# Optimization experiments

Hardware: AMD Instinct MI355X
Metric: run time of the kernel (lower is better)

Reference implementation:

```python
import jax, jax.numpy as jnp
import numpy as np

SE = 128        # num_sensors
T = 256         # timesteps
D_OB = 4        # d_ob_emb
D_PE = 16
D_STATIC = 64
B = 128
N_HEADS = 4
D_FF = 128
N_TRAN = 2
N_PROP = 2
N_CLASSES = 2
D_FEAT = T * D_OB              # 1024, prop-layer feature dim
D_MODEL = SE * D_OB + D_PE     # 528, transformer d_model
D_FINAL = D_MODEL + SE * D_OB  # 1040, mlp input (with static emb)
LN_EPS = 1e-5
NEG_INF = -1e9


def _layernorm(x, g, b):
    m = jnp.mean(x, axis=-1, keepdims=True)
    v = jnp.mean(jnp.square(x - m), axis=-1, keepdims=True)
    return (x - m) * jax.lax.rsqrt(v + LN_EPS) * g + b


def setup_inputs() -> dict:
    key = jax.random.key(0)
    ks = iter(jax.random.split(key, 40))

    def g(shape, scale=0.02):
        return jax.random.normal(next(ks), shape, jnp.float32) * scale

    a = float(np.sqrt(6.0 / (1 + SE * D_OB)))  # glorot for R_u
    inp = {
        'src': jax.random.normal(next(ks), (T, B, 2 * SE), jnp.float32),
        'times': jax.random.uniform(next(ks), (T, B), jnp.float32) * T,
        'lengths': jax.random.randint(next(ks), (B,), 1, T + 1),
        'static': jax.random.normal(next(ks), (B, D_STATIC), jnp.float32),
        'R_u': jax.random.uniform(next(ks), (1, SE * D_OB), jnp.float32, -a, a),
        'static_W': g((SE * D_OB, D_STATIC)),
        'static_b': g((SE * D_OB,)),
        'p_Wq': g((N_PROP, D_FEAT, D_FEAT)),
        'p_Wk': g((N_PROP, D_FEAT, D_FEAT)),
        'p_Wv': g((N_PROP, D_FEAT, D_FEAT)),
        'p_bq': g((N_PROP, D_FEAT)),
        'p_bk': g((N_PROP, D_FEAT)),
        'p_bv': g((N_PROP, D_FEAT)),
        'p_Wskip': g((N_PROP, D_FEAT, D_FEAT)),
        'p_bskip': g((N_PROP, D_FEAT)),
        't_Wqkv': g((N_TRAN, 3 * D_MODEL, D_MODEL)),
        't_bqkv': g((N_TRAN, 3 * D_MODEL)),
        't_Wo': g((N_TRAN, D_MODEL, D_MODEL)),
        't_bo': g((N_TRAN, D_MODEL)),
        't_W1': g((N_TRAN, D_FF, D_MODEL)),
        't_b1': g((N_TRAN, D_FF)),
        't_W2': g((N_TRAN, D_MODEL, D_FF)),
        't_b2': g((N_TRAN, D_MODEL)),
        't_ln1g': jnp.ones((N_TRAN, D_MODEL), jnp.float32),
        't_ln1b': jnp.zeros((N_TRAN, D_MODEL), jnp.float32),
        't_ln2g': jnp.ones((N_TRAN, D_MODEL), jnp.float32),
        't_ln2b': jnp.zeros((N_TRAN, D_MODEL), jnp.float32),
        'mlp_W1': g((D_FINAL, D_FINAL)),
        'mlp_b1': g((D_FINAL,)),
        'mlp_W2': g((N_CLASSES, D_FINAL)),
        'mlp_b2': g((N_CLASSES,)),
    }
    return inp


def reference(src, times, lengths, static, R_u, static_W, static_b,
              p_Wq, p_Wk, p_Wv, p_bq, p_bk, p_bv, p_Wskip, p_bskip,
              t_Wqkv, t_bqkv, t_Wo, t_bo, t_W1, t_b1, t_W2, t_b2,
              t_ln1g, t_ln1b, t_ln2g, t_ln2b,
              mlp_W1, mlp_b1, mlp_W2, mlp_b2):
    # --- positional encoding (PositionalEncodingTF): sin/cos of times over timescales ---
    ts = jnp.asarray(float(T)) ** jnp.linspace(0.0, 1.0, D_PE // 2)
    st = times[..., None] / ts                       # (T,B,D_PE//2)
    pe = jnp.concatenate([jnp.sin(st), jnp.cos(st)], axis=-1)  # (T,B,D_PE)

    static_emb = static @ static_W.T + static_b      # (B, SE*D_OB)

    # --- per-sensor observation embedding ---
    x = src[:, :, :SE]
    x = jnp.repeat(x, D_OB, axis=-1)                 # (T,B,SE*D_OB)
    h = jax.nn.relu(x * R_u)                         # dropout = identity (eval)

    # --- diagonalized graphs: each batch element is a fully-connected Se-node graph.
    # The block-diagonal edge list over B*Se*Se edges is equivalent to dense
    # batched attention (B, Se, Se); we honor that structure densely. ---
    hg = h.reshape(T, B, SE, D_OB).transpose(1, 2, 0, 3).reshape(B, SE, D_FEAT)
    W = jnp.ones((B, SE, SE), h.dtype)               # edge weights [b, tgt, src], adj=ones
    scale = 1.0 / jnp.sqrt(jnp.asarray(D_FEAT, h.dtype))
    for l in range(N_PROP):
        q = hg @ p_Wq[l].T + p_bq[l]
        k = hg @ p_Wk[l].T + p_bk[l]
        v = hg @ p_Wv[l].T + p_bv[l]
        scores = jnp.einsum('bid,bjd->bij', q, k) * scale   # i=target, j=source
        alpha = jax.nn.softmax(scores, axis=-1)              # softmax over sources
        hg = jnp.einsum('bij,bjd->bid', alpha * W, v) + hg @ p_Wskip[l].T + p_bskip[l]
        W = alpha                                            # attn weights feed next layer

    out = hg.reshape(B, SE, T, D_OB).transpose(2, 0, 1, 3).reshape(T, B, SE * D_OB)
    out = jnp.concatenate([out, pe], axis=2)          # (T,B,D_MODEL)

    # --- transformer encoder (post-norm, relu FF, key_padding_mask) ---
    time_mask = jnp.arange(T)[None, :] >= lengths[:, None]   # (B,T) True = pad
    hd = D_MODEL // N_HEADS
    xx = out
    for l in range(N_TRAN):
        qkv = xx @ t_Wqkv[l].T + t_bqkv[l]            # (T,B,3*D_MODEL)
        q, k, v = jnp.split(qkv, 3, axis=-1)
        def _heads(z):
            return z.reshape(T, B, N_HEADS, hd).transpose(1, 2, 0, 3)  # (B,H,T,hd)
        qh, kh, vh = _heads(q), _heads(k), _heads(v)
        att = jnp.einsum('bhqd,bhkd->bhqk', qh, kh) / jnp.sqrt(jnp.asarray(hd, xx.dtype))
        att = jnp.where(time_mask[:, None, None, :], NEG_INF, att)
        att = jax.nn.softmax(att, axis=-1)
        o = jnp.einsum('bhqk,bhkd->bhqd', att, vh).transpose(2, 0, 1, 3).reshape(T, B, D_MODEL)
        o = o @ t_Wo[l].T + t_bo[l]
        xx = _layernorm(xx + o, t_ln1g[l], t_ln1b[l])
        ff = jax.nn.relu(xx @ t_W1[l].T + t_b1[l]) @ t_W2[l].T + t_b2[l]
        xx = _layernorm(xx + ff, t_ln2g[l], t_ln2b[l])

    # --- masked mean pooling over time, static concat, MLP head ---
    keep = (~time_mask).astype(xx.dtype).T[:, :, None]        # (T,B,1)
    pooled = jnp.sum(xx * keep, axis=0) / (lengths[:, None].astype(xx.dtype) + 1.0)
    pooled = jnp.concatenate([pooled, static_emb], axis=1)    # (B, D_FINAL)
    hid = jax.nn.relu(pooled @ mlp_W1.T + mlp_b1)
    return hid @ mlp_W2.T + mlp_b2                            # (B, N_CLASSES)
```

## Files before the change

kernel.cpp:

```cpp
#include <hip/hip_runtime.h>
#include <hip/hip_bf16.h>
#include <math.h>

#define SE_    128
#define T_     256
#define B_     128
#define NH_    4
#define HD_    132
#define D_MODEL_ 528
#define D_FINAL_ 1040
#define D_FF_  128

typedef __hip_bfloat16 bf16;
typedef __attribute__((ext_vector_type(8))) short bf16x8v;
typedef __attribute__((ext_vector_type(4))) float f32x4;

__device__ __forceinline__ float bfb(unsigned short u){
  union { float f; unsigned int i; } c; c.i = ((unsigned int)u) << 16; return c.f;
}
__device__ __forceinline__ unsigned short bfr(float x){
  unsigned u = __builtin_bit_cast(unsigned, x);
  unsigned r = (u + 0x7FFFu + ((u >> 16) & 1u)) >> 16;
  return (unsigned short)r;
}
__device__ __forceinline__ void split1(float x, short& h, short& l){
  const unsigned short hu = bfr(x);
  const unsigned short lu = bfr(x - bfb(hu));
  h = (short)hu; l = (short)lu;
}
__device__ __forceinline__ float prd(const short* p, long i, long lo){
  return bfb((unsigned short)p[i]) + bfb((unsigned short)p[i+lo]);
}
__device__ __forceinline__ float rdIn(const void* p, long i, int f32){
  return f32 ? ((const float*)p)[i] : __bfloat162float(((const bf16*)p)[i]);
}

__global__ void detect_k(const void* __restrict__ src, int* __restrict__ flag){
  const unsigned int* p = (const unsigned int*)src;
  int bad = 0;
  for (int i = threadIdx.x; i < 4096; i += 256){
    const unsigned int lo = p[i] & 0xFFFFu;
    const unsigned int e = (lo >> 7) & 0xFFu;
    if (e >= 0xC0u) bad++;
  }
  __shared__ int red[256];
  red[threadIdx.x] = bad; __syncthreads();
  for (int h = 128; h > 0; h >>= 1){
    if (threadIdx.x < h) red[threadIdx.x] += red[threadIdx.x+h];
    __syncthreads();
  }
  if (threadIdx.x == 0) *flag = (red[0] > 64) ? 1 : 0;
}

#define MAXE 40
struct CvtTab {
  const void* src[MAXE];
  long srcOff[MAXE];
  long dstOff[MAXE];
  int n[MAXE];
  int bstart[MAXE];
  int cnt;
};
__global__ void cvt_all(CvtTab tb, short* __restrict__ wts, long loW, const int* __restrict__ flag){
  const int b = blockIdx.x;
  int e = 0;
  for (int i = 1; i < tb.cnt; ++i) if (tb.bstart[i] <= b) e = i;
  const long i = (long)(b - tb.bstart[e])*256 + threadIdx.x;
  if (i >= tb.n[e]) return;
  const float v = rdIn(tb.src[e], tb.srcOff[e] + i, *flag);
  short h, l; split1(v, h, l);
  wts[tb.dstOff[e] + i] = h;
  wts[tb.dstOff[e] + i + loW] = l;
}

struct RegsP { int4 v[4]; };

template<bool A16>
__device__ __forceinline__ void ld_pair(const short* __restrict__ P, long lo, long ld,
                                        int kb, int K, int g, bool valid, int sc0, RegsP& r){
  short* a = (short*)r.v;
  const int k0 = kb + sc0;
  const short* ph = P + (long)g*ld + k0;
  if (valid && (k0 + 16 <= K)){
    if (A16){
      r.v[0] = *(const int4*)(ph);
      r.v[1] = *(const int4*)(ph + 8);
      r.v[2] = *(const int4*)(ph + lo);
      r.v[3] = *(const int4*)(ph + lo + 8);
    } else {
      #pragma unroll
      for (int q=0;q<4;++q){
        *(int2*)(a + q*4)      = *(const int2*)(ph + q*4);
        *(int2*)(a + 16 + q*4) = *(const int2*)(ph + lo + q*4);
      }
    }
  } else {
    #pragma unroll
    for (int e2=0;e2<16;++e2){
      const bool ok = valid && (k0 + e2 < K);
      a[e2]    = ok ? ph[e2] : (short)0;
      a[16+e2] = ok ? ph[lo + e2] : (short)0;
    }
  }
}

__device__ __forceinline__ void ld_f32(const float* __restrict__ P, long ld, int kb, int K,
                                       int g, bool valid, int sc0, float* f){
  const int k0 = kb + sc0;
  const float* p = P + (long)g*ld + k0;
  if (valid && (k0 + 16 <= K)){
    #pragma unroll
    for (int q=0;q<4;++q) *(float4*)(f+q*4) = *(const float4*)(p + q*4);
  } else {
    #pragma unroll
    for (int e2=0;e2<16;++e2) f[e2] = (valid && (k0+e2) < K) ? p[e2] : 0.f;
  }
}

__device__ __forceinline__ void wr_pair(const RegsP& r, short* Lh, short* Ll, int srow, int sc0){
  *(int4*)(&Lh[srow*40 + sc0])     = r.v[0];
  *(int4*)(&Lh[srow*40 + sc0 + 8]) = r.v[1];
  *(int4*)(&Ll[srow*40 + sc0])     = r.v[2];
  *(int4*)(&Ll[srow*40 + sc0 + 8]) = r.v[3];
}
__device__ __forceinline__ void wr_split(const float* f, short* Lh, short* Ll, int srow, int sc0){
  short h[16], l[16];
  #pragma unroll
  for (int e2=0;e2<16;++e2) split1(f[e2], h[e2], l[e2]);
  *(int4*)(&Lh[srow*40+sc0])   = *(const int4*)(h);
  *(int4*)(&Lh[srow*40+sc0+8]) = *(const int4*)(h+8);
  *(int4*)(&Ll[srow*40+sc0])   = *(const int4*)(l);
  *(int4*)(&Ll[srow*40+sc0+8]) = *(const int4*)(l+8);
}

struct Route { short* C; long ldc; long lo; long sC; long sC2; int nEnd; int fl; };

template<bool SPLITA, bool A16>
__global__ __launch_bounds__(256) void gemm_s(
    const void* __restrict__ Ag, long loA,
    const short* __restrict__ Bg, long loB,
    const short* __restrict__ bias, long loBias,
    int M, int N, int K, long lda, long ldb,
    int nz1, long sA, long sB, long sA2, long sB2,
    int relu, int nroute, Route r0, Route r1, Route r2, float mult)
{
  __shared__ short As_h[128*40], As_l[128*40], Bs_h[128*40], Bs_l[128*40];
  const int tid = threadIdx.x;
  const int z1 = blockIdx.z % nz1, z2 = blockIdx.z / nz1;
  const int m0 = blockIdx.y*128, n0 = blockIdx.x*128;
  const void* A;
  if (SPLITA) A = (const void*)((const float*)Ag + z1*sA + z2*sA2);
  else        A = (const void*)((const short*)Ag + z1*sA + z2*sA2);
  const short* B = Bg + z1*sB + z2*sB2;
  short* Cb0 = r0.C + z1*r0.sC + z2*r0.sC2;
  short* Cb1 = (nroute > 1) ? (r1.C + z1*r1.sC + z2*r1.sC2) : nullptr;
  short* Cb2 = (nroute > 2) ? (r2.C + z1*r2.sC + z2*r2.sC2) : nullptr;

  const int srow = tid >> 1, sc0 = (tid & 1)*16;
  const int lane = tid & 63, wv = tid >> 6;
  const int wm = (wv >> 1)*64, wn = (wv & 1)*64;
  const int fr = lane & 15, kq = (lane >> 4)*8;

  const int gm_s = m0 + srow; const bool mval = gm_s < M;
  const int gn_s = n0 + srow; const bool nval = gn_s < N;

  RegsP rA, rB; float fA[16];
  if (SPLITA) ld_f32((const float*)A, lda, 0, K, gm_s, mval, sc0, fA);
  else        ld_pair<A16>((const short*)A, loA, lda, 0, K, gm_s, mval, sc0, rA);
  ld_pair<A16>(B, loB, ldb, 0, K, gn_s, nval, sc0, rB);

  f32x4 acc[4][4] = {};
  for (int kb = 0; kb < K; kb += 32){
    if (SPLITA) wr_split(fA, As_h, As_l, srow, sc0);
    else        wr_pair(rA, As_h, As_l, srow, sc0);
    wr_pair(rB, Bs_h, Bs_l, srow, sc0);
    __syncthreads();
    const int kn = kb + 32;
    if (kn < K){
      if (SPLITA) ld_f32((const float*)A, lda, kn, K, gm_s, mval, sc0, fA);
      else        ld_pair<A16>((const short*)A, loA, lda, kn, K, gm_s, mval, sc0, rA);
      ld_pair<A16>(B, loB, ldb, kn, K, gn_s, nval, sc0, rB);
    }
    bf16x8v ah[4], al[4], bh[4], bl[4];
    #pragma unroll
    for (int i=0;i<4;++i){
      ah[i] = *reinterpret_cast<const bf16x8v*>(&As_h[(wm + i*16 + fr)*40 + kq]);
      al[i] = *reinterpret_cast<const bf16x8v*>(&As_l[(wm + i*16 + fr)*40 + kq]);
      bh[i] = *reinterpret_cast<const bf16x8v*>(&Bs_h[(wn + i*16 + fr)*40 + kq]);
      bl[i] = *reinterpret_cast<const bf16x8v*>(&Bs_l[(wn + i*16 + fr)*40 + kq]);
    }
    #pragma unroll
    for (int i=0;i<4;++i)
      #pragma unroll
      for (int j=0;j<4;++j){
        acc[i][j] = __builtin_amdgcn_mfma_f32_16x16x32_bf16(ah[i], bh[j], acc[i][j], 0,0,0);
        acc[i][j] = __builtin_amdgcn_mfma_f32_16x16x32_bf16(ah[i], bl[j], acc[i][j], 0,0,0);
        acc[i][j] = __builtin_amdgcn_mfma_f32_16x16x32_bf16(al[i], bh[j], acc[i][j], 0,0,0);
      }
    __syncthreads();
  }

  const int cr = (lane >> 4)*4, cc = lane & 15;
  #pragma unroll
  for (int i=0;i<4;++i){
    #pragma unroll
    for (int j=0;j<4;++j){
      #pragma unroll
      for (int rr=0;rr<4;++rr){
        const int gm = m0 + wm + i*16 + cr + rr;
        const int gn = n0 + wn + j*16 + cc;
        if (gm < M && gn < N){
          float v = acc[i][j][rr] * mult;
          if (bias) v += prd(bias, gn, loBias);
          if (relu) v = fmaxf(v, 0.f);
          short* Cp; long ldc, lo; int fl, cn;
          if (nroute > 1 && gn >= r0.nEnd){
            if (nroute > 2 && gn >= r1.nEnd){ Cp=Cb2; ldc=r2.ldc; lo=r2.lo; fl=r2.fl; cn=gn-r1.nEnd; }
            else                            { Cp=Cb1; ldc=r1.ldc; lo=r1.lo; fl=r1.fl; cn=gn-r0.nEnd; }
          } else                            { Cp=Cb0; ldc=r0.ldc; lo=r0.lo; fl=r0.fl; cn=gn; }
          const long idx = (fl & 1) ? ((long)cn*ldc + gm) : ((long)gm*ldc + cn);
          if (fl & 2) v += prd(Cp, idx, lo);
          short h, l; split1(v, h, l);
          Cp[idx] = h; Cp[idx + lo] = l;
        }
      }
    }
  }
}

template<int NN, bool A16>
__global__ __launch_bounds__(256) void gemm_sm(
    const short* __restrict__ Ag, long loA, const short* __restrict__ Bg, long loB,
    int K, long lda, long ldb,
    int nz1, long sA, long sB, long sA2, long sB2,
    float* __restrict__ Sg, long sS, long sS2, int ldS,
    float mult, const int* __restrict__ lengths, int b0,
    const float* __restrict__ mulP, long sMul)
{
  __shared__ short As_h[128*40], As_l[128*40], Bs_h[128*40], Bs_l[128*40];
  const int tid = threadIdx.x;
  const int z1 = blockIdx.z % nz1, z2 = blockIdx.z / nz1;
  const int m0 = blockIdx.y*128;
  const short* A = Ag + z1*sA + z2*sA2;
  const short* B = Bg + z1*sB + z2*sB2;
  float* S = Sg + z1*sS + z2*sS2;

  const int srow = tid >> 1, sc0 = (tid & 1)*16;
  const int lane = tid & 63, wv = tid >> 6;
  const int wm = (wv >> 1)*64, wn = (wv & 1)*64;
  const int fr = lane & 15, kq = (lane >> 4)*8;
  const int cr = (lane >> 4)*4, cc = lane & 15;

  for (int nh = 0; nh < NN; nh += 128){
    RegsP rA, rB;
    ld_pair<A16>(A, loA, lda, 0, K, m0+srow, true, sc0, rA);
    ld_pair<A16>(B, loB, ldb, 0, K, nh+srow, true, sc0, rB);
    f32x4 acc[4][4] = {};
    for (int kb = 0; kb < K; kb += 32){
      wr_pair(rA, As_h, As_l, srow, sc0);
      wr_pair(rB, Bs_h, Bs_l, srow, sc0);
      __syncthreads();
      const int kn = kb + 32;
      if (kn < K){
        ld_pair<A16>(A, loA, lda, kn, K, m0+srow, true, sc0, rA);
        ld_pair<A16>(B, loB, ldb, kn, K, nh+srow, true, sc0, rB);
      }
      bf16x8v ah[4], al[4], bh[4], bl[4];
      #pragma unroll
      for (int i=0;i<4;++i){
        ah[i] = *reinterpret_cast<const bf16x8v*>(&As_h[(wm + i*16 + fr)*40 + kq]);
        al[i] = *reinterpret_cast<const bf16x8v*>(&As_l[(wm + i*16 + fr)*40 + kq]);
        bh[i] = *reinterpret_cast<const bf16x8v*>(&Bs_h[(wn + i*16 + fr)*40 + kq]);
        bl[i] = *reinterpret_cast<const bf16x8v*>(&Bs_l[(wn + i*16 + fr)*40 + kq]);
      }
      #pragma unroll
      for (int i=0;i<4;++i)
        #pragma unroll
        for (int j=0;j<4;++j){
          acc[i][j] = __builtin_amdgcn_mfma_f32_16x16x32_bf16(ah[i], bh[j], acc[i][j], 0,0,0);
          acc[i][j] = __builtin_amdgcn_mfma_f32_16x16x32_bf16(ah[i], bl[j], acc[i][j], 0,0,0);
          acc[i][j] = __builtin_amdgcn_mfma_f32_16x16x32_bf16(al[i], bh[j], acc[i][j], 0,0,0);
        }
      __syncthreads();
    }
    #pragma unroll
    for (int i=0;i<4;++i)
      #pragma unroll
      for (int j=0;j<4;++j)
        #pragma unroll
        for (int rr=0;rr<4;++rr){
          const int gm = m0 + wm + i*16 + cr + rr;
          const int gn = nh + wn + j*16 + cc;
          S[(long)gm*ldS + gn] = acc[i][j][rr] * mult;
        }
  }
  __syncthreads();

  constexpr int CH = NN / 64;
  const int cbase = lane*CH;
  int lim = NN;
  if (lengths){ const int L = lengths[b0 + z1]; lim = (L < NN) ? L : NN; }

  float v[CH], vn[CH], mcur[CH], mnxt[CH];
  {
    float* row0 = S + (long)(m0 + wv*32)*ldS + cbase;
    #pragma unroll
    for (int e=0;e<CH;++e) v[e] = row0[e];
    if (mulP){
      const float* mr = mulP + z1*sMul + (long)(m0 + wv*32)*ldS + cbase;
      #pragma unroll
      for (int e=0;e<CH;++e) mcur[e] = mr[e];
    }
  }
  for (int i = 0; i < 32; ++i){
    if (i < 31){
      float* rn = S + (long)(m0 + wv*32 + i + 1)*ldS + cbase;
      #pragma unroll
      for (int e=0;e<CH;++e) vn[e] = rn[e];
      if (mulP){
        const float* mr = mulP + z1*sMul + (long)(m0 + wv*32 + i + 1)*ldS + cbase;
        #pragma unroll
        for (int e=0;e<CH;++e) mnxt[e] = mr[e];
      }
    }
    float mx = -3.0e38f;
    #pragma unroll
    for (int e=0;e<CH;++e) if (cbase+e < lim) mx = fmaxf(mx, v[e]);
    #pragma unroll
    for (int o=32;o>0;o>>=1) mx = fmaxf(mx, __shfl_xor(mx, o, 64));
    float sm = 0.f;
    #pragma unroll
    for (int e=0;e<CH;++e){
      v[e] = (cbase+e < lim) ? __expf(v[e] - mx) : 0.f;
      sm += v[e];
    }
    #pragma unroll
    for (int o=32;o>0;o>>=1) sm += __shfl_xor(sm, o, 64);
    const float inv = 1.f / sm;
    float* row = S + (long)(m0 + wv*32 + i)*ldS + cbase;
    if (mulP){
      #pragma unroll
      for (int e=0;e<CH;++e) row[e] = v[e]*inv*mcur[e];
    } else {
      #pragma unroll
      for (int e=0;e<CH;++e) row[e] = v[e]*inv;
    }
    #pragma unroll
    for (int e=0;e<CH;++e){ v[e] = vn[e]; mcur[e] = mnxt[e]; }
  }
}

__global__ void build_hg(const void* __restrict__ src, const short* __restrict__ Ru, long loW,
                         short* __restrict__ hg, long loH, const int* __restrict__ flag, int b0){
  const int t = blockIdx.x, bl = blockIdx.y, se = threadIdx.x;
  const int f32 = *flag;
  const float s = rdIn(src, ((long)t*B_ + (b0+bl))*(2*SE_) + se, f32);
  const long o = ((long)bl*SE_ + se)*1024 + t*4;
  #pragma unroll
  for (int j=0;j<4;++j){
    const float v = fmaxf(s * prd(Ru, se*4+j, loW), 0.f);
    short h, l; split1(v, h, l);
    hg[o+j] = h; hg[o+j+loH] = l;
  }
}

__global__ void build_xx(const short* __restrict__ hg, long loH,
                         const short* __restrict__ times, long loW,
                         short* __restrict__ xx, long loX, int b0, int G){
  const int blk = blockIdx.x;
  const int t = blk / G, bl = blk % G, b = b0 + bl;
  const int tid = threadIdx.x;
  const float tm = prd(times, (long)t*B_ + b, loW);
  for (int c = tid; c < D_MODEL_; c += 256){
    float v;
    if (c < SE_*4){
      v = prd(hg, ((long)bl*SE_ + (c>>2))*1024 + t*4 + (c&3), loH);
    } else {
      const int p = c - SE_*4;
      const int i = p & 7;
      const float ts = exp2f(8.0f * (float)i / 7.0f);
      const float st = tm / ts;
      v = (p < 8) ? sinf(st) : cosf(st);
    }
    short h, l; split1(v, h, l);
    const long o = ((long)t*B_ + b)*D_MODEL_ + c;
    xx[o] = h; xx[o+loX] = l;
  }
}

__device__ __forceinline__ void ln_body_p(short* px, long loX, const short* pr, long loR,
                                          const short* g, const short* bb, long loW, int tid){
  const float x0 = prd(px,tid,loX)     + prd(pr,tid,loR);
  const float x1 = prd(px,tid+256,loX) + prd(pr,tid+256,loR);
  const float x2 = (tid < 16) ? (prd(px,tid+512,loX) + prd(pr,tid+512,loR)) : 0.f;
  __shared__ float rs[256], rq[256];
  rs[tid] = x0 + x1 + x2;
  rq[tid] = x0*x0 + x1*x1 + x2*x2;
  __syncthreads();
  for (int h = 128; h > 0; h >>= 1){
    if (tid < h){ rs[tid] += rs[tid+h]; rq[tid] += rq[tid+h]; }
    __syncthreads();
  }
  const float mean = rs[0] * (1.0f/528.0f);
  const float var  = rq[0] * (1.0f/528.0f) - mean*mean;
  const float inv = rsqrtf(var + 1e-5f);
  short h, l;
  split1((x0-mean)*inv*prd(g,tid,loW) + prd(bb,tid,loW), h, l);
  px[tid] = h; px[tid+loX] = l;
  split1((x1-mean)*inv*prd(g,tid+256,loW) + prd(bb,tid+256,loW), h, l);
  px[tid+256] = h; px[tid+256+loX] = l;
  if (tid < 16){
    split1((x2-mean)*inv*prd(g,tid+512,loW) + prd(bb,tid+512,loW), h, l);
    px[tid+512] = h; px[tid+512+loX] = l;
  }
}

__global__ __launch_bounds__(256) void ln_res_attn(short* __restrict__ xx, long loX,
    const short* __restrict__ res, long loR,
    const short* __restrict__ g, const short* __restrict__ bb, long loW, int b0){
  const int z = blockIdx.x >> 8, t = blockIdx.x & 255;
  short* px = xx + ((long)t*B_ + b0 + z)*D_MODEL_;
  const short* pr = res + (long)blockIdx.x*D_MODEL_;
  ln_body_p(px, loX, pr, loR, g, bb, loW, threadIdx.x);
}

__global__ __launch_bounds__(256) void ln_res_rows(short* __restrict__ xx, long loX,
    const short* __restrict__ res, long loR,
    const short* __restrict__ g, const short* __restrict__ bb, long loW, int r0){
  short* px = xx + ((long)r0 + blockIdx.x)*D_MODEL_;
  const short* pr = res + (long)blockIdx.x*D_MODEL_;
  ln_body_p(px, loX, pr, loR, g, bb, loW, threadIdx.x);
}

__global__ void pool_k(const short* __restrict__ xx, long loX, const int* __restrict__ len,
                       short* __restrict__ pooled, long loP){
  const int b = blockIdx.y;
  const int c = blockIdx.x*256 + threadIdx.x;
  if (c >= D_MODEL_) return;
  const int L = len[b];
  float s = 0.f;
  for (int t = 0; t < L; ++t) s += prd(xx, ((long)t*B_ + b)*D_MODEL_ + c, loX);
  short h, l; split1(s / (float)(L + 1), h, l);
  pooled[(long)b*D_FINAL_ + c] = h;
  pooled[(long)b*D_FINAL_ + c + loP] = l;
}

__global__ void logits_k(const short* __restrict__ hid, long loH,
                         const short* __restrict__ W2, const short* __restrict__ b2, long loW,
                         void* __restrict__ out, const int* __restrict__ flag){
  const int z = blockIdx.x;
  const int b = z >> 1, c = z & 1;
  const int lane = threadIdx.x;
  float s = 0.f;
  for (int k = lane; k < D_FINAL_; k += 64)
    s += prd(hid, (long)b*D_FINAL_ + k, loH) * prd(W2, (long)c*D_FINAL_ + k, loW);
  #pragma unroll
  for (int o = 32; o > 0; o >>= 1) s += __shfl_down(s, o, 64);
  if (lane == 0){
    const float r = s + prd(b2, c, loW);
    if (*flag) ((float*)out)[z] = r;
    else       ((bf16*)out)[z] = __float2bfloat16(r);
  }
}

extern "C" void kernel_launch(void* const* d_in, const int* in_sizes, int n_in,
                              void* d_out, int out_size, void* d_ws, size_t ws_size,
                              hipStream_t stream) {
  const int* lengths = (const int*)d_in[2];
  char* ws = (char*)d_ws;
  const size_t KB = 1024;

  short* wtsH = (short*)ws;
  int* flag = (int*)(ws + 47500*KB);
  short* xxH = (short*)(ws + 48000*KB);
  const long loXX = 17301504;
  char* SC = ws + 115600*KB;

  short* hgA = (short*)(SC + 0*KB);      const long loHG = 2097152;
  short* hgB = (short*)(SC + 8192*KB);
  short* qkc = (short*)(SC + 16384*KB);  const long loQK1 = 4194304;
  short* VtS = (short*)(SC + 32768*KB);  const long loVT1 = 2097152;
  float* S0c = (float*)(SC + 40960*KB);
  float* S1c = (float*)(SC + 41984*KB);
  short* qkb = (short*)(SC + 0*KB);      const long loQK2 = 4325376;
  short* o_c = (short*)(SC + 0*KB);      const long loOC  = 2162688;
  short* pjb = (short*)(SC + 8448*KB);   const long loPJ  = 2162688;
  short* vtb = (short*)(SC + 16896*KB);  const long loVT2 = 2162688;
  float* att = (float*)(SC + 25344*KB);
  short* ff1 = (short*)(SC + 0*KB);      const long loFF  = 4194304;
  short* pj2 = (short*)(SC + 16896*KB);  const long loPJ2 = 4325376;
  short* pooled = (short*)(SC + 0*KB);   const long loPO  = 133120;
  short* hid    = (short*)(SC + 1024*KB);

  CvtTab tb; long cur = 0; int nb = 0; int e = 0;
  auto add = [&](int idx, long so, long n)->long{
    tb.src[e] = d_in[idx]; tb.srcOff[e] = so; tb.dstOff[e] = cur;
    tb.n[e] = (int)n; tb.bstart[e] = nb;
    nb += (int)((n + 255)/256); cur += n; e++;
    return cur - n;
  };
  const long oT  = add(1,0,32768);
  const long oSt = add(3,0,8192);
  const long oRu = add(4,0,512);
  const long oSW = add(5,0,32768);
  const long oSb = add(6,0,512);
  long oQKSV[2], oBQ[2];
  for (int l = 0; l < 2; ++l){
    oQKSV[l] = add(7, (long)l*1048576, 1048576);
    add(8,  (long)l*1048576, 1048576);
    add(13, (long)l*1048576, 1048576);
    add(9,  (long)l*1048576, 1048576);
  }
  for (int l = 0; l < 2; ++l){
    oBQ[l] = add(10, (long)l*1024, 1024);
    add(11, (long)l*1024, 1024);
    add(14, (long)l*1024, 1024);
    add(12, (long)l*1024, 1024);
  }
  const long oWqkv = add(15,0,1672704);
  const long obqkv = add(16,0,3168);
  const long oWo = add(17,0,557568);
  const long obo = add(18,0,1056);
  const long oW1 = add(19,0,135168);
  const long ob1 = add(20,0,256);
  const long oW2 = add(21,0,135168);
  const long ob2 = add(22,0,1056);
  const long og1 = add(23,0,1056);
  const long obb1 = add(24,0,1056);
  const long og2 = add(25,0,1056);
  const long obb2 = add(26,0,1056);
  const long oM1 = add(27,0,1081600);
  const long oM1b = add(28,0,1040);
  const long oM2 = add(29,0,2080);
  const long oM2b = add(30,0,2);
  tb.cnt = e;
  const long loW = (cur + 7) & ~7L;

  detect_k<<<1,256,0,stream>>>(d_in[0], flag);
  cvt_all<<<nb,256,0,stream>>>(tb, wtsH, loW, flag);

  const Route RZ{nullptr,0,0,0,0,0,0};

  const int G1 = 16;
  for (int b0 = 0; b0 < B_; b0 += G1){
    build_hg<<<dim3(T_, G1), 128, 0, stream>>>(d_in[0], wtsH+oRu, loW, hgA, loHG, flag, b0);
    short* curb = hgA; short* nxtb = hgB;
    for (int l = 0; l < 2; ++l){
      float* S = (l == 0) ? S0c : S1c;
      {
        Route q{qkc, 2048, loQK1, 0, 0, 2048, 0};
        Route s{nxtb, 1024, loHG, 0, 0, 3072, 0};
        Route v{VtS, 2048, loVT1, 0, 0, 4096, 1};
        gemm_s<false,true><<<dim3(32,16,1),256,0,stream>>>(
            curb, loHG, wtsH+oQKSV[l], loW, wtsH+oBQ[l], loW,
            2048, 4096, 1024, 1024, 1024,
            1, 0,0,0,0, 0, 3, q, s, v, 1.f);
      }
      gemm_sm<128,true><<<dim3(1,1,G1),256,0,stream>>>(
          qkc, loQK1, qkc+1024, loQK1,
          1024, 2048, 2048,
          G1, 262144, 262144, 0, 0,
          S, 16384, 0, 128,
          0.03125f, nullptr, 0,
          (l == 1) ? S0c : nullptr, 16384);
      {
        Route c{nxtb, 1024, loHG, 131072, 0, 1024, 2};
        gemm_s<true,true><<<dim3(8,1,G1),256,0,stream>>>(
            S, 0, VtS, loVT1, nullptr, 0,
            128, 1024, 128, 128, 2048,
            G1, 16384, 128, 0, 0, 0, 1, c, RZ, RZ, 1.f);
      }
      short* t_ = curb; curb = nxtb; nxtb = t_;
    }
    build_xx<<<T_*G1,256,0,stream>>>(curb, loHG, wtsH+oT, loW, xxH, loXX, b0, G1);
  }

  const float iscl = 1.0f / sqrtf((float)HD_);
  const int G2 = 16;
  for (int l = 0; l < 2; ++l){
    const long wqkv = oWqkv + (long)l*836352;
    const long bqkv = obqkv + (long)l*1584;
    for (int b0 = 0; b0 < B_; b0 += G2){
      {
        Route qk{qkb, 1056, loQK2, 270336, 0, 1056, 0};
        Route v{vtb, 256, loVT2, 135168, 0, 1584, 1};
        gemm_s<false,true><<<dim3(13,2,G2),256,0,stream>>>(
            xxH + (long)b0*D_MODEL_, loXX, wtsH+wqkv, loW, wtsH+bqkv, loW,
            256, 1584, 528, (long)B_*D_MODEL_, 528,
            G2, 528, 0, 0, 0, 0, 2, qk, v, RZ, 1.f);
      }
      gemm_sm<256,false><<<dim3(1,2,G2*NH_),256,0,stream>>>(
          qkb, loQK2, qkb+528, loQK2,
          132, 1056, 1056,
          G2, 270336, 270336, 132, 132,
          att, 262144, 65536, 256,
          iscl, lengths, b0, nullptr, 0);
      {
        Route c{o_c, 528, loOC, 135168, 132, HD_, 0};
        gemm_s<true,true><<<dim3(2,2,G2*NH_),256,0,stream>>>(
            att, 0, vtb, loVT2, nullptr, 0,
            256, HD_, 256, 256, 256,
            G2, 262144, 135168, 65536, 33792, 0, 1, c, RZ, RZ, 1.f);
      }
      {
        Route c{pjb, 528, loPJ, 135168, 0, 528, 0};
        gemm_s<false,true><<<dim3(5,2,G2),256,0,stream>>>(
            o_c, loOC, wtsH+oWo+(long)l*278784, loW, wtsH+obo+(long)l*528, loW,
            256, 528, 528, 528, 528,
            G2, 135168, 0, 0, 0, 0, 1, c, RZ, RZ, 1.f);
      }
      ln_res_attn<<<G2*256,256,0,stream>>>(xxH, loXX, pjb, loPJ,
          wtsH+og1+(long)l*528, wtsH+obb1+(long)l*528, loW, b0);
    }
    {
      Route c{ff1, 128, loFF, 0, 0, 128, 0};
      gemm_s<false,true><<<dim3(1,256,1),256,0,stream>>>(
          xxH, loXX, wtsH+oW1+(long)l*67584, loW, wtsH+ob1+(long)l*128, loW,
          32768, 128, 528, 528, 528,
          1, 0,0,0,0, 1, 1, c, RZ, RZ, 1.f);
    }
    for (int r0 = 0; r0 < 32768; r0 += 8192){
      Route c{pj2, 528, loPJ2, 0, 0, 528, 0};
      gemm_s<false,true><<<dim3(5,64,1),256,0,stream>>>(
          ff1 + (long)r0*128, loFF, wtsH+oW2+(long)l*67584, loW, wtsH+ob2+(long)l*528, loW,
          8192, 528, 128, 128, 128,
          1, 0,0,0,0, 0, 1, c, RZ, RZ, 1.f);
      ln_res_rows<<<8192,256,0,stream>>>(xxH, loXX, pj2, loPJ2,
          wtsH+og2+(long)l*528, wtsH+obb2+(long)l*528, loW, r0);
    }
  }

  pool_k<<<dim3(3,B_),256,0,stream>>>(xxH, loXX, lengths, pooled, loPO);
  {
    Route c{pooled + D_MODEL_, 1040, loPO, 0, 0, 512, 0};
    gemm_s<false,true><<<dim3(4,1,1),256,0,stream>>>(
        wtsH+oSt, loW, wtsH+oSW, loW, wtsH+oSb, loW,
        128, 512, 64, 64, 64,
        1, 0,0,0,0, 0, 1, c, RZ, RZ, 1.f);
  }
  {
    Route c{hid, 1040, loPO, 0, 0, 1040, 0};
    gemm_s<false,true><<<dim3(9,1,1),256,0,stream>>>(
        pooled, loPO, wtsH+oM1, loW, wtsH+oM1b, loW,
        128, 1040, 1040, 1040, 1040,
        1, 0,0,0,0, 1, 1, c, RZ, RZ, 1.f);
  }
  logits_k<<<B_*2,64,0,stream>>>(hid, loPO, wtsH+oM2, wtsH+oM2b, loW, d_out, flag);
}
```

Baseline: 7.323 ms.

## Load GEMM B-operand fragments directly from global into registers, bypassing LDS

Both GEMM kernels now read each wave's B fragments straight from global memory into registers, double-buffered across k-steps, instead of staging B through shared memory. This halves LDS usage and LDS traffic per block and removes the B writes before each barrier, which could allow higher occupancy. In exchange, the two waves that share a B column range each load it separately, so global/L2 traffic for B doubles. Loads are also less coalesced (16-byte rows strided by ldb), and the two-deep register buffers raise register pressure.

```diff
diff --git a/kernel.cpp b/kernel.cpp
--- a/kernel.cpp
+++ b/kernel.cpp
@@ -133,9 +133,40 @@
   *(int4*)(&Ll[srow*40+sc0+8]) = *(const int4*)(l+8);
 }
 
+template<int DB>
+__device__ __forceinline__ void ldB_frag(const short* __restrict__ Bf, long lo, long ldb,
+                                         int kb, int K, int N, int nbase, int fr, int kq,
+                                         int4 bh[4], int4 bl[4]){
+  const int k0 = kb + kq;
+  #pragma unroll
+  for (int j=0;j<4;++j){
+    int gn = nbase + j*16 + fr;
+    if (gn >= N) gn = N-1;
+    const short* p = Bf + (long)gn*ldb + k0;
+    if (k0 + 8 <= K){
+      if (DB == 16){
+        bh[j] = *(const int4*)(p);
+        bl[j] = *(const int4*)(p + lo);
+      } else {
+        int2* h2 = (int2*)&bh[j]; int2* l2 = (int2*)&bl[j];
+        h2[0] = *(const int2*)(p);      h2[1] = *(const int2*)(p + 4);
+        l2[0] = *(const int2*)(p + lo); l2[1] = *(const int2*)(p + lo + 4);
+      }
+    } else {
+      short* hs = (short*)&bh[j]; short* ls = (short*)&bl[j];
+      #pragma unroll
+      for (int e=0;e<8;++e){
+        const bool ok = (k0 + e) < K;
+        hs[e] = ok ? p[e] : (short)0;
+        ls[e] = ok ? p[lo + e] : (short)0;
+      }
+    }
+  }
+}
+
 struct Route { short* C; long ldc; long lo; long sC; long sC2; int nEnd; int fl; };
 
-template<bool SPLITA, bool A16>
+template<bool SPLITA, bool A16, int DB>
 __global__ __launch_bounds__(256) void gemm_s(
     const void* __restrict__ Ag, long loA,
     const short* __restrict__ Bg, long loB,
@@ -144,7 +175,7 @@
     int nz1, long sA, long sB, long sA2, long sB2,
     int relu, int nroute, Route r0, Route r1, Route r2, float mult)
 {
-  __shared__ short As_h[128*40], As_l[128*40], Bs_h[128*40], Bs_l[128*40];
+  __shared__ short As_h[128*40], As_l[128*40];
   const int tid = threadIdx.x;
   const int z1 = blockIdx.z % nz1, z2 = blockIdx.z / nz1;
   const int m0 = blockIdx.y*128, n0 = blockIdx.x*128;
@@ -162,40 +193,40 @@
   const int fr = lane & 15, kq = (lane >> 4)*8;
 
   const int gm_s = m0 + srow; const bool mval = gm_s < M;
-  const int gn_s = n0 + srow; const bool nval = gn_s < N;
-
-  RegsP rA, rB; float fA[16];
+
+  RegsP rA; float fA[16];
   if (SPLITA) ld_f32((const float*)A, lda, 0, K, gm_s, mval, sc0, fA);
   else        ld_pair<A16>((const short*)A, loA, lda, 0, K, gm_s, mval, sc0, rA);
-  ld_pair<A16>(B, loB, ldb, 0, K, gn_s, nval, sc0, rB);
+  int4 bhv[2][4], blv[2][4];
+  ldB_frag<DB>(B, loB, ldb, 0, K, N, n0+wn, fr, kq, bhv[0], blv[0]);
 
   f32x4 acc[4][4] = {};
-  for (int kb = 0; kb < K; kb += 32){
+  int p = 0;
+  for (int kb = 0; kb < K; kb += 32, p ^= 1){
     if (SPLITA) wr_split(fA, As_h, As_l, srow, sc0);
     else        wr_pair(rA, As_h, As_l, srow, sc0);
-    wr_pair(rB, Bs_h, Bs_l, srow, sc0);
     __syncthreads();
     const int kn = kb + 32;
     if (kn < K){
       if (SPLITA) ld_f32((const float*)A, lda, kn, K, gm_s, mval, sc0, fA);
       else        ld_pair<A16>((const short*)A, loA, lda, kn, K, gm_s, mval, sc0, rA);
-      ld_pair<A16>(B, loB, ldb, kn, K, gn_s, nval, sc0, rB);
-    }
-    bf16x8v ah[4], al[4], bh[4], bl[4];
+      ldB_frag<DB>(B, loB, ldb, kn, K, N, n0+wn, fr, kq, bhv[p^1], blv[p^1]);
+    }
+    bf16x8v ah[4], al[4];
     #pragma unroll
     for (int i=0;i<4;++i){
       ah[i] = *reinterpret_cast<const bf16x8v*>(&As_h[(wm + i*16 + fr)*40 + kq]);
       al[i] = *reinterpret_cast<const bf16x8v*>(&As_l[(wm + i*16 + fr)*40 + kq]);
-      bh[i] = *reinterpret_cast<const bf16x8v*>(&Bs_h[(wn + i*16 + fr)*40 + kq]);
-      bl[i] = *reinterpret_cast<const bf16x8v*>(&Bs_l[(wn + i*16 + fr)*40 + kq]);
     }
     #pragma unroll
     for (int i=0;i<4;++i)
       #pragma unroll
       for (int j=0;j<4;++j){
-        acc[i][j] = __builtin_amdgcn_mfma_f32_16x16x32_bf16(ah[i], bh[j], acc[i][j], 0,0,0);
-        acc[i][j] = __builtin_amdgcn_mfma_f32_16x16x32_bf16(ah[i], bl[j], acc[i][j], 0,0,0);
-        acc[i][j] = __builtin_amdgcn_mfma_f32_16x16x32_bf16(al[i], bh[j], acc[i][j], 0,0,0);
+        const bf16x8v bh = __builtin_bit_cast(bf16x8v, bhv[p][j]);
+        const bf16x8v bl = __builtin_bit_cast(bf16x8v, blv[p][j]);
+        acc[i][j] = __builtin_amdgcn_mfma_f32_16x16x32_bf16(ah[i], bh, acc[i][j], 0,0,0);
+        acc[i][j] = __builtin_amdgcn_mfma_f32_16x16x32_bf16(ah[i], bl, acc[i][j], 0,0,0);
+        acc[i][j] = __builtin_amdgcn_mfma_f32_16x16x32_bf16(al[i], bh, acc[i][j], 0,0,0);
       }
     __syncthreads();
   }
@@ -228,7 +259,7 @@
   }
 }
 
-template<int NN, bool A16>
+template<int NN, bool A16, int DB>
 __global__ __launch_bounds__(256) void gemm_sm(
     const short* __restrict__ Ag, long loA, const short* __restrict__ Bg, long loB,
     int K, long lda, long ldb,
@@ -237,7 +268,7 @@
     float mult, const int* __restrict__ lengths, int b0,
     const float* __restrict__ mulP, long sMul)
 {
-  __shared__ short As_h[128*40], As_l[128*40], Bs_h[128*40], Bs_l[128*40];
+  __shared__ short As_h[128*40], As_l[128*40];
   const int tid = threadIdx.x;
   const int z1 = blockIdx.z % nz1, z2 = blockIdx.z / nz1;
   const int m0 = blockIdx.y*128;
@@ -252,34 +283,35 @@
   const int cr = (lane >> 4)*4, cc = lane & 15;
 
   for (int nh = 0; nh < NN; nh += 128){
-    RegsP rA, rB;
+    RegsP rA;
     ld_pair<A16>(A, loA, lda, 0, K, m0+srow, true, sc0, rA);
-    ld_pair<A16>(B, loB, ldb, 0, K, nh+srow, true, sc0, rB);
+    int4 bhv[2][4], blv[2][4];
+    ldB_frag<DB>(B, loB, ldb, 0, K, NN, nh+wn, fr, kq, bhv[0], blv[0]);
     f32x4 acc[4][4] = {};
-    for (int kb = 0; kb < K; kb += 32){
+    int p = 0;
+    for (int kb = 0; kb < K; kb += 32, p ^= 1){
       wr_pair(rA, As_h, As_l, srow, sc0);
-      wr_pair(rB, Bs_h, Bs_l, srow, sc0);
       __syncthreads();
       const int kn = kb + 32;
       if (kn < K){
         ld_pair<A16>(A, loA, lda, kn, K, m0+srow, true, sc0, rA);
-        ld_pair<A16>(B, loB, ldb, kn, K, nh+srow, true, sc0, rB);
-      }
-      bf16x8v ah[4], al[4], bh[4], bl[4];
+        ldB_frag<DB>(B, loB, ldb, kn, K, NN, nh+wn, fr, kq, bhv[p^1], blv[p^1]);
+      }
+      bf16x8v ah[4], al[4];
       #pragma unroll
       for (int i=0;i<4;++i){
         ah[i] = *reinterpret_cast<const bf16x8v*>(&As_h[(wm + i*16 + fr)*40 + kq]);
         al[i] = *reinterpret_cast<const bf16x8v*>(&As_l[(wm + i*16 + fr)*40 + kq]);
-        bh[i] = *reinterpret_cast<const bf16x8v*>(&Bs_h[(wn + i*16 + fr)*40 + kq]);
-        bl[i] = *reinterpret_cast<const bf16x8v*>(&Bs_l[(wn + i*16 + fr)*40 + kq]);
       }
       #pragma unroll
       for (int i=0;i<4;++i)
         #pragma unroll
         for (int j=0;j<4;++j){
-          acc[i][j] = __builtin_amdgcn_mfma_f32_16x16x32_bf16(ah[i], bh[j], acc[i][j], 0,0,0);
-          acc[i][j] = __builtin_amdgcn_mfma_f32_16x16x32_bf16(ah[i], bl[j], acc[i][j], 0,0,0);
-          acc[i][j] = __builtin_amdgcn_mfma_f32_16x16x32_bf16(al[i], bh[j], acc[i][j], 0,0,0);
+          const bf16x8v bh = __builtin_bit_cast(bf16x8v, bhv[p][j]);
+          const bf16x8v bl = __builtin_bit_cast(bf16x8v, blv[p][j]);
+          acc[i][j] = __builtin_amdgcn_mfma_f32_16x16x32_bf16(ah[i], bh, acc[i][j], 0,0,0);
+          acc[i][j] = __builtin_amdgcn_mfma_f32_16x16x32_bf16(ah[i], bl, acc[i][j], 0,0,0);
+          acc[i][j] = __builtin_amdgcn_mfma_f32_16x16x32_bf16(al[i], bh, acc[i][j], 0,0,0);
         }
       __syncthreads();
     }
@@ -551,12 +583,12 @@
         Route q{qkc, 2048, loQK1, 0, 0, 2048, 0};
         Route s{nxtb, 1024, loHG, 0, 0, 3072, 0};
         Route v{VtS, 2048, loVT1, 0, 0, 4096, 1};
-        gemm_s<false,true><<<dim3(32,16,1),256,0,stream>>>(
+        gemm_s<false,true,16><<<dim3(32,16,1),256,0,stream>>>(
             curb, loHG, wtsH+oQKSV[l], loW, wtsH+oBQ[l], loW,
             2048, 4096, 1024, 1024, 1024,
             1, 0,0,0,0, 0, 3, q, s, v, 1.f);
       }
-      gemm_sm<128,true><<<dim3(1,1,G1),256,0,stream>>>(
+      gemm_sm<128,true,16><<<dim3(1,1,G1),256,0,stream>>>(
           qkc, loQK1, qkc+1024, loQK1,
           1024, 2048, 2048,
           G1, 262144, 262144, 0, 0,
@@ -565,7 +597,7 @@
           (l == 1) ? S0c : nullptr, 16384);
       {
         Route c{nxtb, 1024, loHG, 131072, 0, 1024, 2};
-        gemm_s<true,true><<<dim3(8,1,G1),256,0,stream>>>(
+        gemm_s<true,true,16><<<dim3(8,1,G1),256,0,stream>>>(
             S, 0, VtS, loVT1, nullptr, 0,
             128, 1024, 128, 128, 2048,
             G1, 16384, 128, 0, 0, 0, 1, c, RZ, RZ, 1.f);
@@ -584,12 +616,12 @@
       {
         Route qk{qkb, 1056, loQK2, 270336, 0, 1056, 0};
         Route v{vtb, 256, loVT2, 135168, 0, 1584, 1};
-        gemm_s<false,true><<<dim3(13,2,G2),256,0,stream>>>(
+        gemm_s<false,true,16><<<dim3(13,2,G2),256,0,stream>>>(
             xxH + (long)b0*D_MODEL_, loXX, wtsH+wqkv, loW, wtsH+bqkv, loW,
             256, 1584, 528, (long)B_*D_MODEL_, 528,
             G2, 528, 0, 0, 0, 0, 2, qk, v, RZ, 1.f);
       }
-      gemm_sm<256,false><<<dim3(1,2,G2*NH_),256,0,stream>>>(
+      gemm_sm<256,false,8><<<dim3(1,2,G2*NH_),256,0,stream>>>(
           qkb, loQK2, qkb+528, loQK2,
           132, 1056, 1056,
           G2, 270336, 270336, 132, 132,
@@ -597,14 +629,14 @@
           iscl, lengths, b0, nullptr, 0);
       {
         Route c{o_c, 528, loOC, 135168, 132, HD_, 0};
-        gemm_s<true,true><<<dim3(2,2,G2*NH_),256,0,stream>>>(
+        gemm_s<true,true,16><<<dim3(2,2,G2*NH_),256,0,stream>>>(
             att, 0, vtb, loVT2, nullptr, 0,
             256, HD_, 256, 256, 256,
             G2, 262144, 135168, 65536, 33792, 0, 1, c, RZ, RZ, 1.f);
       }
       {
         Route c{pjb, 528, loPJ, 135168, 0, 528, 0};
-        gemm_s<false,true><<<dim3(5,2,G2),256,0,stream>>>(
+        gemm_s<false,true,16><<<dim3(5,2,G2),256,0,stream>>>(
             o_c, loOC, wtsH+oWo+(long)l*278784, loW, wtsH+obo+(long)l*528, loW,
             256, 528, 528, 528, 528,
             G2, 135168, 0, 0, 0, 0, 1, c, RZ, RZ, 1.f);
@@ -614,14 +646,14 @@
     }
     {
       Route c{ff1, 128, loFF, 0, 0, 128, 0};
-      gemm_s<false,true><<<dim3(1,256,1),256,0,stream>>>(
+      gemm_s<false,true,16><<<dim3(1,256,1),256,0,stream>>>(
           xxH, loXX, wtsH+oW1+(long)l*67584, loW, wtsH+ob1+(long)l*128, loW,
           32768, 128, 528, 528, 528,
           1, 0,0,0,0, 1, 1, c, RZ, RZ, 1.f);
     }
     for (int r0 = 0; r0 < 32768; r0 += 8192){
       Route c{pj2, 528, loPJ2, 0, 0, 528, 0};
-      gemm_s<false,true><<<dim3(5,64,1),256,0,stream>>>(
+      gemm_s<false,true,16><<<dim3(5,64,1),256,0,stream>>>(
           ff1 + (long)r0*128, loFF, wtsH+oW2+(long)l*67584, loW, wtsH+ob2+(long)l*528, loW,
           8192, 528, 128, 128, 128,
           1, 0,0,0,0, 0, 1, c, RZ, RZ, 1.f);
@@ -633,14 +665,14 @@
   pool_k<<<dim3(3,B_),256,0,stream>>>(xxH, loXX, lengths, pooled, loPO);
   {
     Route c{pooled + D_MODEL_, 1040, loPO, 0, 0, 512, 0};
-    gemm_s<false,true><<<dim3(4,1,1),256,0,stream>>>(
+    gemm_s<false,true,16><<<dim3(4,1,1),256,0,stream>>>(
         wtsH+oSt, loW, wtsH+oSW, loW, wtsH+oSb, loW,
         128, 512, 64, 64, 64,
         1, 0,0,0,0, 0, 1, c, RZ, RZ, 1.f);
   }
   {
     Route c{hid, 1040, loPO, 0, 0, 1040, 0};
-    gemm_s<false,true><<<dim3(9,1,1),256,0,stream>>>(
+    gemm_s<false,true,16><<<dim3(9,1,1),256,0,stream>>>(
         pooled, loPO, wtsH+oM1, loW, wtsH+oM1b, loW,
         128, 1040, 1040, 1040, 1040,
         1, 0,0,0,0, 1, 1, c, RZ, RZ, 1.f);
```

Result: slower. 13.74 ms (+87.7%).

## Stage GEMM tiles via direct global-to-LDS loads with XOR-swizzled shared layout

Applied to the files above, without the earlier changes.

Replaces register-staged, padded LDS tiles in the split-bf16 GEMM kernels with direct global_load_lds transfers into an unpadded, XOR-swizzled 32-wide layout. A register fallback path handles K tails and fp32 A inputs. LDS per block shrinks, launch bounds now request two blocks per CU, and the MFMA loop order is swapped. The goal is less VGPR traffic and fewer LDS bank conflicts, but the register prefetch of the next K tile is dropped, so loads are no longer overlapped with the MFMAs. Rows past the edge are clamped, not zeroed.

```diff
diff --git a/kernel.cpp b/kernel.cpp
--- a/kernel.cpp
+++ b/kernel.cpp
@@ -73,70 +73,102 @@
   wts[tb.dstOff[e] + i + loW] = l;
 }
 
-struct RegsP { int4 v[4]; };
-
-template<bool A16>
-__device__ __forceinline__ void ld_pair(const short* __restrict__ P, long lo, long ld,
-                                        int kb, int K, int g, bool valid, int sc0, RegsP& r){
-  short* a = (short*)r.v;
-  const int k0 = kb + sc0;
-  const short* ph = P + (long)g*ld + k0;
-  if (valid && (k0 + 16 <= K)){
-    if (A16){
-      r.v[0] = *(const int4*)(ph);
-      r.v[1] = *(const int4*)(ph + 8);
-      r.v[2] = *(const int4*)(ph + lo);
-      r.v[3] = *(const int4*)(ph + lo + 8);
+__device__ __forceinline__ int swz(int r){ return (r&3) ^ ((r>>2)&3); }
+
+__device__ __forceinline__ void gllstage_pair(const short* __restrict__ g, long lo, long ld,
+    int kb, int row_g0, int rmax, int tid, short* Lh, short* Ll){
+  const int w = tid>>6, ln = tid&63;
+  #pragma unroll
+  for (int inst=0; inst<2; ++inst){
+    const int r = (w*2+inst)*16 + (ln>>2);
+    int gr = row_g0 + r; if (gr > rmax) gr = rmax;
+    const int q = (ln&3) ^ (((ln>>2)&3) ^ ((ln>>4)&3));
+    const short* p = g + (long)gr*ld + kb + q*8;
+    short* dh = Lh + (w*2+inst)*512;
+    short* dl = Ll + (w*2+inst)*512;
+    __builtin_amdgcn_global_load_lds(
+        (const __attribute__((address_space(1))) void*)p,
+        (__attribute__((address_space(3))) void*)dh, 16, 0, 0);
+    __builtin_amdgcn_global_load_lds(
+        (const __attribute__((address_space(1))) void*)(p + lo),
+        (__attribute__((address_space(3))) void*)dl, 16, 0, 0);
+  }
+}
+
+__device__ __forceinline__ void regstage_pair(const short* __restrict__ g, long lo, long ld,
+    int kb, int K, int row_g0, int rmax, int tid, short* Lh, short* Ll){
+  const int r = tid>>1;
+  int gr = row_g0 + r; if (gr > rmax) gr = rmax;
+  const int s = swz(r);
+  #pragma unroll
+  for (int cq=0;cq<2;++cq){
+    const int q = (tid&1)*2 + cq;
+    const int k0 = kb + q*8;
+    short bh[8], bl[8];
+    const short* p = g + (long)gr*ld + k0;
+    if (k0 + 8 <= K){
+      *(int2*)(bh)   = *(const int2*)(p);      *(int2*)(bh+4) = *(const int2*)(p+4);
+      *(int2*)(bl)   = *(const int2*)(p+lo);   *(int2*)(bl+4) = *(const int2*)(p+lo+4);
     } else {
       #pragma unroll
-      for (int q=0;q<4;++q){
-        *(int2*)(a + q*4)      = *(const int2*)(ph + q*4);
-        *(int2*)(a + 16 + q*4) = *(const int2*)(ph + lo + q*4);
-      }
-    }
-  } else {
-    #pragma unroll
-    for (int e2=0;e2<16;++e2){
-      const bool ok = valid && (k0 + e2 < K);
-      a[e2]    = ok ? ph[e2] : (short)0;
-      a[16+e2] = ok ? ph[lo + e2] : (short)0;
-    }
-  }
-}
-
-__device__ __forceinline__ void ld_f32(const float* __restrict__ P, long ld, int kb, int K,
-                                       int g, bool valid, int sc0, float* f){
-  const int k0 = kb + sc0;
-  const float* p = P + (long)g*ld + k0;
-  if (valid && (k0 + 16 <= K)){
-    #pragma unroll
-    for (int q=0;q<4;++q) *(float4*)(f+q*4) = *(const float4*)(p + q*4);
-  } else {
-    #pragma unroll
-    for (int e2=0;e2<16;++e2) f[e2] = (valid && (k0+e2) < K) ? p[e2] : 0.f;
-  }
-}
-
-__device__ __forceinline__ void wr_pair(const RegsP& r, short* Lh, short* Ll, int srow, int sc0){
-  *(int4*)(&Lh[srow*40 + sc0])     = r.v[0];
-  *(int4*)(&Lh[srow*40 + sc0 + 8]) = r.v[1];
-  *(int4*)(&Ll[srow*40 + sc0])     = r.v[2];
-  *(int4*)(&Ll[srow*40 + sc0 + 8]) = r.v[3];
-}
-__device__ __forceinline__ void wr_split(const float* f, short* Lh, short* Ll, int srow, int sc0){
-  short h[16], l[16];
+      for (int e=0;e<8;++e){
+        const bool ok = (k0+e) < K;
+        bh[e] = ok ? p[e] : (short)0;
+        bl[e] = ok ? p[lo+e] : (short)0;
+      }
+    }
+    const int c = q ^ s;
+    *(int4*)&Lh[r*32 + c*8] = *(const int4*)bh;
+    *(int4*)&Ll[r*32 + c*8] = *(const int4*)bl;
+  }
+}
+
+__device__ __forceinline__ void regstage_f32(const float* __restrict__ g, long ld,
+    int kb, int K, int row_g0, int rmax, int tid, short* Lh, short* Ll){
+  const int r = tid>>1;
+  int gr = row_g0 + r; if (gr > rmax) gr = rmax;
+  const int s = swz(r);
   #pragma unroll
-  for (int e2=0;e2<16;++e2) split1(f[e2], h[e2], l[e2]);
-  *(int4*)(&Lh[srow*40+sc0])   = *(const int4*)(h);
-  *(int4*)(&Lh[srow*40+sc0+8]) = *(const int4*)(h+8);
-  *(int4*)(&Ll[srow*40+sc0])   = *(const int4*)(l);
-  *(int4*)(&Ll[srow*40+sc0+8]) = *(const int4*)(l+8);
+  for (int cq=0;cq<2;++cq){
+    const int q = (tid&1)*2 + cq;
+    const int k0 = kb + q*8;
+    short bh[8], bl[8];
+    const float* p = g + (long)gr*ld + k0;
+    if (k0 + 8 <= K){
+      float f[8];
+      *(float4*)(f)   = *(const float4*)(p);
+      *(float4*)(f+4) = *(const float4*)(p+4);
+      #pragma unroll
+      for (int e=0;e<8;++e) split1(f[e], bh[e], bl[e]);
+    } else {
+      #pragma unroll
+      for (int e=0;e<8;++e){
+        const float v = (k0+e < K) ? p[e] : 0.f;
+        split1(v, bh[e], bl[e]);
+      }
+    }
+    const int c = q ^ s;
+    *(int4*)&Lh[r*32 + c*8] = *(const int4*)bh;
+    *(int4*)&Ll[r*32 + c*8] = *(const int4*)bl;
+  }
+}
+
+__device__ __forceinline__ void rd_frags(const short* Lh, const short* Ll,
+                                         int wbase, int fr, int qlog,
+                                         bf16x8v ah[4], bf16x8v al[4]){
+  const int cs = (qlog ^ ((fr&3) ^ ((fr>>2)&3))) * 8;
+  #pragma unroll
+  for (int i=0;i<4;++i){
+    const int r_ = wbase + i*16 + fr;
+    ah[i] = *reinterpret_cast<const bf16x8v*>(&Lh[r_*32 + cs]);
+    al[i] = *reinterpret_cast<const bf16x8v*>(&Ll[r_*32 + cs]);
+  }
 }
 
 struct Route { short* C; long ldc; long lo; long sC; long sC2; int nEnd; int fl; };
 
-template<bool SPLITA, bool A16>
-__global__ __launch_bounds__(256) void gemm_s(
+template<bool SPLITA, bool GLL>
+__global__ __launch_bounds__(256, 2) void gemm_s(
     const void* __restrict__ Ag, long loA,
     const short* __restrict__ Bg, long loB,
     const short* __restrict__ bias, long loBias,
@@ -144,7 +176,7 @@
     int nz1, long sA, long sB, long sA2, long sB2,
     int relu, int nroute, Route r0, Route r1, Route r2, float mult)
 {
-  __shared__ short As_h[128*40], As_l[128*40], Bs_h[128*40], Bs_l[128*40];
+  __shared__ short As_h[128*32], As_l[128*32], Bs_h[128*32], Bs_l[128*32];
   const int tid = threadIdx.x;
   const int z1 = blockIdx.z % nz1, z2 = blockIdx.z / nz1;
   const int m0 = blockIdx.y*128, n0 = blockIdx.x*128;
@@ -156,43 +188,27 @@
   short* Cb1 = (nroute > 1) ? (r1.C + z1*r1.sC + z2*r1.sC2) : nullptr;
   short* Cb2 = (nroute > 2) ? (r2.C + z1*r2.sC + z2*r2.sC2) : nullptr;
 
-  const int srow = tid >> 1, sc0 = (tid & 1)*16;
   const int lane = tid & 63, wv = tid >> 6;
   const int wm = (wv >> 1)*64, wn = (wv & 1)*64;
-  const int fr = lane & 15, kq = (lane >> 4)*8;
-
-  const int gm_s = m0 + srow; const bool mval = gm_s < M;
-  const int gn_s = n0 + srow; const bool nval = gn_s < N;
-
-  RegsP rA, rB; float fA[16];
-  if (SPLITA) ld_f32((const float*)A, lda, 0, K, gm_s, mval, sc0, fA);
-  else        ld_pair<A16>((const short*)A, loA, lda, 0, K, gm_s, mval, sc0, rA);
-  ld_pair<A16>(B, loB, ldb, 0, K, gn_s, nval, sc0, rB);
+  const int fr = lane & 15, qlog = lane >> 4;
 
   f32x4 acc[4][4] = {};
   for (int kb = 0; kb < K; kb += 32){
-    if (SPLITA) wr_split(fA, As_h, As_l, srow, sc0);
-    else        wr_pair(rA, As_h, As_l, srow, sc0);
-    wr_pair(rB, Bs_h, Bs_l, srow, sc0);
+    const bool tail = (kb + 32 > K);
+    if (SPLITA) regstage_f32((const float*)A, lda, kb, K, m0, M-1, tid, As_h, As_l);
+    else if (GLL && !tail) gllstage_pair((const short*)A, loA, lda, kb, m0, M-1, tid, As_h, As_l);
+    else regstage_pair((const short*)A, loA, lda, kb, K, m0, M-1, tid, As_h, As_l);
+    if (GLL && !tail) gllstage_pair(B, loB, ldb, kb, n0, N-1, tid, Bs_h, Bs_l);
+    else regstage_pair(B, loB, ldb, kb, K, n0, N-1, tid, Bs_h, Bs_l);
     __syncthreads();
-    const int kn = kb + 32;
-    if (kn < K){
-      if (SPLITA) ld_f32((const float*)A, lda, kn, K, gm_s, mval, sc0, fA);
-      else        ld_pair<A16>((const short*)A, loA, lda, kn, K, gm_s, mval, sc0, rA);
-      ld_pair<A16>(B, loB, ldb, kn, K, gn_s, nval, sc0, rB);
-    }
+
     bf16x8v ah[4], al[4], bh[4], bl[4];
-    #pragma unroll
-    for (int i=0;i<4;++i){
-      ah[i] = *reinterpret_cast<const bf16x8v*>(&As_h[(wm + i*16 + fr)*40 + kq]);
-      al[i] = *reinterpret_cast<const bf16x8v*>(&As_l[(wm + i*16 + fr)*40 + kq]);
-      bh[i] = *reinterpret_cast<const bf16x8v*>(&Bs_h[(wn + i*16 + fr)*40 + kq]);
-      bl[i] = *reinterpret_cast<const bf16x8v*>(&Bs_l[(wn + i*16 + fr)*40 + kq]);
-    }
-    #pragma unroll
-    for (int i=0;i<4;++i)
-      #pragma unroll
-      for (int j=0;j<4;++j){
+    rd_frags(As_h, As_l, wm, fr, qlog, ah, al);
+    rd_frags(Bs_h, Bs_l, wn, fr, qlog, bh, bl);
+    #pragma unroll
+    for (int j=0;j<4;++j)
+      #pragma unroll
+      for (int i=0;i<4;++i){
         acc[i][j] = __builtin_amdgcn_mfma_f32_16x16x32_bf16(ah[i], bh[j], acc[i][j], 0,0,0);
         acc[i][j] = __builtin_amdgcn_mfma_f32_16x16x32_bf16(ah[i], bl[j], acc[i][j], 0,0,0);
         acc[i][j] = __builtin_amdgcn_mfma_f32_16x16x32_bf16(al[i], bh[j], acc[i][j], 0,0,0);
@@ -228,8 +244,8 @@
   }
 }
 
-template<int NN, bool A16>
-__global__ __launch_bounds__(256) void gemm_sm(
+template<int NN, bool GLL>
+__global__ __launch_bounds__(256, 2) void gemm_sm(
     const short* __restrict__ Ag, long loA, const short* __restrict__ Bg, long loB,
     int K, long lda, long ldb,
     int nz1, long sA, long sB, long sA2, long sB2,
@@ -237,7 +253,7 @@
     float mult, const int* __restrict__ lengths, int b0,
     const float* __restrict__ mulP, long sMul)
 {
-  __shared__ short As_h[128*40], As_l[128*40], Bs_h[128*40], Bs_l[128*40];
+  __shared__ short As_h[128*32], As_l[128*32], Bs_h[128*32], Bs_l[128*32];
   const int tid = threadIdx.x;
   const int z1 = blockIdx.z % nz1, z2 = blockIdx.z / nz1;
   const int m0 = blockIdx.y*128;
@@ -245,38 +261,30 @@
   const short* B = Bg + z1*sB + z2*sB2;
   float* S = Sg + z1*sS + z2*sS2;
 
-  const int srow = tid >> 1, sc0 = (tid & 1)*16;
   const int lane = tid & 63, wv = tid >> 6;
   const int wm = (wv >> 1)*64, wn = (wv & 1)*64;
-  const int fr = lane & 15, kq = (lane >> 4)*8;
+  const int fr = lane & 15, qlog = lane >> 4;
   const int cr = (lane >> 4)*4, cc = lane & 15;
 
   for (int nh = 0; nh < NN; nh += 128){
-    RegsP rA, rB;
-    ld_pair<A16>(A, loA, lda, 0, K, m0+srow, true, sc0, rA);
-    ld_pair<A16>(B, loB, ldb, 0, K, nh+srow, true, sc0, rB);
     f32x4 acc[4][4] = {};
     for (int kb = 0; kb < K; kb += 32){
-      wr_pair(rA, As_h, As_l, srow, sc0);
-      wr_pair(rB, Bs_h, Bs_l, srow, sc0);
+      const bool tail = (kb + 32 > K);
+      if (GLL && !tail){
+        gllstage_pair(A, loA, lda, kb, m0, m0+127, tid, As_h, As_l);
+        gllstage_pair(B, loB, ldb, kb, nh, nh+127, tid, Bs_h, Bs_l);
+      } else {
+        regstage_pair(A, loA, lda, kb, K, m0, m0+127, tid, As_h, As_l);
+        regstage_pair(B, loB, ldb, kb, K, nh, nh+127, tid, Bs_h, Bs_l);
+      }
       __syncthreads();
-      const int kn = kb + 32;
-      if (kn < K){
-        ld_pair<A16>(A, loA, lda, kn, K, m0+srow, true, sc0, rA);
-        ld_pair<A16>(B, loB, ldb, kn, K, nh+srow, true, sc0, rB);
-      }
       bf16x8v ah[4], al[4], bh[4], bl[4];
-      #pragma unroll
-      for (int i=0;i<4;++i){
-        ah[i] = *reinterpret_cast<const bf16x8v*>(&As_h[(wm + i*16 + fr)*40 + kq]);
-        al[i] = *reinterpret_cast<const bf16x8v*>(&As_l[(wm + i*16 + fr)*40 + kq]);
-        bh[i] = *reinterpret_cast<const bf16x8v*>(&Bs_h[(wn + i*16 + fr)*40 + kq]);
-        bl[i] = *reinterpret_cast<const bf16x8v*>(&Bs_l[(wn + i*16 + fr)*40 + kq]);
-      }
-      #pragma unroll
-      for (int i=0;i<4;++i)
+      rd_frags(As_h, As_l, wm, fr, qlog, ah, al);
+      rd_frags(Bs_h, Bs_l, wn, fr, qlog, bh, bl);
+      #pragma unroll
+      for (int j=0;j<4;++j)
         #pragma unroll
-        for (int j=0;j<4;++j){
+        for (int i=0;i<4;++i){
           acc[i][j] = __builtin_amdgcn_mfma_f32_16x16x32_bf16(ah[i], bh[j], acc[i][j], 0,0,0);
           acc[i][j] = __builtin_amdgcn_mfma_f32_16x16x32_bf16(ah[i], bl[j], acc[i][j], 0,0,0);
           acc[i][j] = __builtin_amdgcn_mfma_f32_16x16x32_bf16(al[i], bh[j], acc[i][j], 0,0,0);
```

After: 7.114 ms. 2.8% less time.
